# Kernel tuning notes

Hardware: AMD Instinct MI355X
Metric: run time of the kernel (lower is better)

The kernel has to match this reference:

```python
import jax, jax.numpy as jnp
import numpy as np

B, LVS, WIDTH, DEPTH = 8192, 512, 512, 7
EPS = 1e-5
SLOPE = 0.01  # torch LeakyReLU default negative_slope


def setup_inputs() -> dict:
    key = jax.random.key(0)
    ks = jax.random.split(key, 16)
    inp = {"x": jax.random.normal(ks[0], (B, LVS), dtype=jnp.float32)}
    for i in range(DEPTH):
        fan_in = LVS + WIDTH * i
        inp[f"W{i}"] = jax.random.normal(ks[1 + i], (WIDTH, fan_in), dtype=jnp.float32) / np.sqrt(fan_in)
    inp["b"] = 0.01 * jax.random.normal(ks[8], (DEPTH, WIDTH), dtype=jnp.float32)
    inp["gamma"] = jnp.ones((DEPTH, WIDTH), dtype=jnp.float32)
    inp["beta"] = jnp.zeros((DEPTH, WIDTH), dtype=jnp.float32)
    cin = LVS + DEPTH * WIDTH  # 4096
    inp["Wc"] = jax.random.normal(ks[9], (1, cin), dtype=jnp.float32) / np.sqrt(cin)
    inp["bc"] = jnp.zeros((1,), dtype=jnp.float32)
    # torch: rv = randn(...) * 0.02 + 1, multiplied onto each projection
    inp["noise"] = 1.0 + 0.02 * jax.random.normal(ks[10], (DEPTH, B, WIDTH), dtype=jnp.float32)
    return inp


def reference(x, W0, W1, W2, W3, W4, W5, W6, b, gamma, beta, Wc, bc, noise):
    Ws = (W0, W1, W2, W3, W4, W5, W6)
    last = x
    for i in range(DEPTH):
        # Linear: [B, in_i] @ [in_i, width]
        h = jnp.einsum('bi,wi->bw', last, Ws[i]) + b[i]
        # BatchNorm1d (training mode: batch stats, biased variance)
        mean = jnp.mean(h, axis=0)
        var = jnp.mean(jnp.square(h - mean), axis=0)
        h = (h - mean) * jax.lax.rsqrt(var + EPS) * gamma[i] + beta[i]
        # LeakyReLU + multiplicative noise, fused elementwise
        h = jnp.where(h >= 0, h, SLOPE * h) * noise[i]
        last = jnp.concatenate((last, h), axis=-1)
    logits = jnp.einsum('bi,oi->bo', last, Wc) + bc
    return jax.nn.sigmoid(logits)
```

## Files before the change

### kernel.cpp

```cpp
#include <hip/hip_runtime.h>

#define B_ROWS 8192
#define WIDTH  512
#define DEPTH  7
#define CIN    4096
#define EPS    1e-5f
#define SLOPE  0.01f

typedef __attribute__((ext_vector_type(8))) short short8;
typedef __attribute__((ext_vector_type(4))) short short4v;
typedef __attribute__((ext_vector_type(4))) float f32x4;
typedef __attribute__((ext_vector_type(16))) float f32x16;

__device__ inline short f2bf(float f) {
  unsigned u = __builtin_bit_cast(unsigned, f);
  unsigned r = (u + 0x7FFFu + ((u >> 16) & 1u)) >> 16;
  return (short)r;
}

__device__ inline float bf2f(short b) {
  unsigned u = ((unsigned)(unsigned short)b) << 16;
  return __builtin_bit_cast(float, u);
}

__device__ inline void gl_lds16(const void* g, void* l) {
  __builtin_amdgcn_global_load_lds(
      (const __attribute__((address_space(1))) unsigned*)g,
      (__attribute__((address_space(3))) unsigned*)l, 16, 0, 0);
}

struct WP { const float* p[7]; };

__global__ __launch_bounds__(256) void prolog(WP wp, short* __restrict__ wbf,
                                              const float* __restrict__ x,
                                              const float* __restrict__ wc,
                                              short* __restrict__ lastbf,
                                              float* __restrict__ logit,
                                              float* __restrict__ sumsz) {
  if (blockIdx.x >= 2048) {
    long e = ((long)(blockIdx.x - 2048) * 256 + threadIdx.x) * 4;
    int layer; long base;
    if      (e < 262144L)  { layer = 0; base = 0; }
    else if (e < 786432L)  { layer = 1; base = 262144L; }
    else if (e < 1572864L) { layer = 2; base = 786432L; }
    else if (e < 2621440L) { layer = 3; base = 1572864L; }
    else if (e < 3932160L) { layer = 4; base = 2621440L; }
    else if (e < 5505024L) { layer = 5; base = 3932160L; }
    else                   { layer = 6; base = 5505024L; }
    f32x4 v = *(const f32x4*)(wp.p[layer] + (e - base));
    short4v o;
    o.x = f2bf(v.x); o.y = f2bf(v.y); o.z = f2bf(v.z); o.w = f2bf(v.w);
    *(short4v*)(wbf + e) = o;
    return;
  }
  int gid = blockIdx.x * 256 + threadIdx.x;
  if (gid < DEPTH * 1024) sumsz[gid] = 0.f;
  int w = threadIdx.x >> 6, l = threadIdx.x & 63;
  int r = blockIdx.x * 4 + w;
  const float* xr = x + (long)r * 512 + l * 8;
  f32x4 v0 = *(const f32x4*)xr;
  f32x4 v1 = *(const f32x4*)(xr + 4);
  const float* wcr = wc + l * 8;
  float acc = 0.f;
  short8 ob;
#pragma unroll
  for (int j = 0; j < 4; ++j) { acc += v0[j] * wcr[j];     ob[j]     = f2bf(v0[j]); }
#pragma unroll
  for (int j = 0; j < 4; ++j) { acc += v1[j] * wcr[4 + j]; ob[4 + j] = f2bf(v1[j]); }
  *(short8*)&lastbf[(long)r * CIN + l * 8] = ob;
#pragma unroll
  for (int off = 32; off; off >>= 1) acc += __shfl_xor(acc, off);
  if (l == 0) logit[r] = acc;
}

__global__ __launch_bounds__(256, 2) void gemm_fused(const short* __restrict__ A,
                                                     const short* __restrict__ Bw,
                                                     short* __restrict__ C,
                                                     float* __restrict__ sums,
                                                     int K) {
  __shared__ __align__(16) char smem[49152];
  int t = threadIdx.x;
  int ks = t >> 6, l = t & 63;
  int l31 = l & 31, hi = l >> 5;
  int bm = blockIdx.x, bn = blockIdx.y;
  const short* Ab = A + (long)(bm * 128) * CIN;
  const short* Bb = Bw + (long)(bn * 64) * K;

  f32x16 acc[4][2];
#pragma unroll
  for (int m = 0; m < 4; ++m)
#pragma unroll
    for (int n = 0; n < 2; ++n)
#pragma unroll
      for (int r = 0; r < 16; ++r) acc[m][n][r] = 0.f;

  int l8 = l >> 3;
  int scol = ((l & 7) ^ l8) << 3;

#define STAGE(buf, k0)                                                                       \
  {                                                                                          \
    char* base = smem + (buf) * 24576;                                                       \
    int c0 = ks * 4, c1 = ks * 2;                                                            \
    gl_lds16(Ab + (long)((c0    ) * 8 + l8) * CIN + (k0) + scol, base + (c0    ) * 1024);    \
    gl_lds16(Ab + (long)((c0 + 1) * 8 + l8) * CIN + (k0) + scol, base + (c0 + 1) * 1024);    \
    gl_lds16(Ab + (long)((c0 + 2) * 8 + l8) * CIN + (k0) + scol, base + (c0 + 2) * 1024);    \
    gl_lds16(Ab + (long)((c0 + 3) * 8 + l8) * CIN + (k0) + scol, base + (c0 + 3) * 1024);    \
    gl_lds16(Bb + (long)((c1    ) * 8 + l8) * K + (k0) + scol, base + 16384 + (c1    ) * 1024); \
    gl_lds16(Bb + (long)((c1 + 1) * 8 + l8) * K + (k0) + scol, base + 16384 + (c1 + 1) * 1024); \
  }

  STAGE(0, 0);
  __syncthreads();

  int kb = ks * 32 + hi * 16;
  int sw = (l & 7) << 4;

  int nt = K >> 6;
  int cur = 0;
  for (int tix = 0; tix < nt; ++tix) {
    if (tix + 1 < nt) STAGE(cur ^ 1, (tix + 1) << 6);
    const char* AsC = smem + cur * 24576;
    const char* BsC = AsC + 16384;
    short8 a[4], b[2];
#pragma unroll
    for (int m = 0; m < 4; ++m)
      a[m] = *(const short8*)(AsC + (m * 32 + l31) * 128 + (kb ^ sw));
#pragma unroll
    for (int n = 0; n < 2; ++n)
      b[n] = *(const short8*)(BsC + (n * 32 + l31) * 128 + (kb ^ sw));
#pragma unroll
    for (int m = 0; m < 4; ++m)
#pragma unroll
      for (int n = 0; n < 2; ++n)
        acc[m][n] = __builtin_amdgcn_mfma_f32_32x32x16_bf16(a[m], b[n], acc[m][n], 0, 0, 0);
    __syncthreads();
    cur ^= 1;
  }

  float* Red = (float*)smem;
#define RIDX(m, n, r) (((m) * 32 + ((r) & 3) + 8 * ((r) >> 2) + 4 * hi) * 64 + (n) * 32 + l31)
  if (ks == 3) {
#pragma unroll
    for (int m = 0; m < 4; ++m)
#pragma unroll
      for (int n = 0; n < 2; ++n)
#pragma unroll
        for (int r = 0; r < 16; ++r) Red[RIDX(m, n, r)] = acc[m][n][r];
  }
  __syncthreads();
  if (ks == 2) {
#pragma unroll
    for (int m = 0; m < 4; ++m)
#pragma unroll
      for (int n = 0; n < 2; ++n)
#pragma unroll
        for (int r = 0; r < 16; ++r) Red[RIDX(m, n, r)] += acc[m][n][r];
  }
  __syncthreads();
  if (ks == 1) {
#pragma unroll
    for (int m = 0; m < 4; ++m)
#pragma unroll
      for (int n = 0; n < 2; ++n)
#pragma unroll
        for (int r = 0; r < 16; ++r) Red[RIDX(m, n, r)] += acc[m][n][r];
  }
  __syncthreads();
  if (ks == 0) {
    short* Cb = C + (long)(bm * 128) * WIDTH + bn * 64;
#pragma unroll
    for (int n = 0; n < 2; ++n) {
      float s = 0.f, q = 0.f;
#pragma unroll
      for (int m = 0; m < 4; ++m) {
#pragma unroll
        for (int r = 0; r < 16; ++r) {
          int cr = (r & 3) + 8 * (r >> 2) + 4 * hi;
          float v = acc[m][n][r] + Red[RIDX(m, n, r)];
          Cb[(long)(m * 32 + cr) * WIDTH + n * 32 + l31] = f2bf(v);
          s += v; q += v * v;
        }
      }
      s += __shfl_xor(s, 32);
      q += __shfl_xor(q, 32);
      if (l < 32) {
        int colg = bn * 64 + n * 32 + l;
        atomicAdd(&sums[colg], s);
        atomicAdd(&sums[WIDTH + colg], q);
      }
    }
  }
#undef RIDX
#undef STAGE
}

__global__ __launch_bounds__(256) void bnact(const short* __restrict__ h,
                                             const float* __restrict__ sums,
                                             const float* __restrict__ gamma,
                                             const float* __restrict__ beta,
                                             const float* __restrict__ noise,
                                             const float* __restrict__ wc,
                                             short* __restrict__ lastseg,
                                             float* __restrict__ logit) {
  int w = threadIdx.x >> 6, l = threadIdx.x & 63;
  int r = blockIdx.x * 4 + w;
  int c = l * 8;
  const float invB = 1.0f / 8192.0f;
  short8 hb = *(const short8*)&h[(long)r * WIDTH + c];
  f32x4 n0 = *(const f32x4*)&noise[(long)r * WIDTH + c];
  f32x4 n1 = *(const f32x4*)&noise[(long)r * WIDTH + c + 4];
  float acc = 0.f;
  short8 ob;
#pragma unroll
  for (int j = 0; j < 8; ++j) {
    int cc = c + j;
    float hv = bf2f(hb[j]);
    float nv = j < 4 ? n0[j] : n1[j - 4];
    float mean = sums[cc] * invB;
    float var = sums[WIDTH + cc] * invB - mean * mean;
    float v = (hv - mean) * rsqrtf(var + EPS);
    v = v * gamma[cc] + beta[cc];
    v = v >= 0.f ? v : SLOPE * v;
    v *= nv;
    acc += v * wc[cc];
    ob[j] = f2bf(v);
  }
  *(short8*)&lastseg[(long)r * CIN + c] = ob;
#pragma unroll
  for (int off = 32; off; off >>= 1) acc += __shfl_xor(acc, off);
  if (l == 0) logit[r] += acc;
}

__global__ __launch_bounds__(256) void finalize(const float* __restrict__ logit,
                                                const float* __restrict__ bc,
                                                float* __restrict__ out) {
  int i = blockIdx.x * 256 + threadIdx.x;
  float z = logit[i] + bc[0];
  out[i] = 1.0f / (1.0f + expf(-z));
}

extern "C" void kernel_launch(void* const* d_in, const int* in_sizes, int n_in,
                              void* d_out, int out_size, void* d_ws, size_t ws_size,
                              hipStream_t stream) {
  (void)in_sizes; (void)n_in; (void)out_size; (void)ws_size;
  const float* x     = (const float*)d_in[0];
  WP wp;
  for (int i = 0; i < 7; ++i) wp.p[i] = (const float*)d_in[1 + i];
  const float* gamma = (const float*)d_in[9];
  const float* beta  = (const float*)d_in[10];
  const float* Wc    = (const float*)d_in[11];
  const float* bc    = (const float*)d_in[12];
  const float* noise = (const float*)d_in[13];

  char* ws = (char*)d_ws;
  short* lastbf = (short*)ws;
  short* hpre   = (short*)(ws + 67108864);
  short* wbf    = (short*)(ws + 67108864 + 16777216);
  float* sums   = (float*)(ws + 67108864 + 16777216 + 14680064);
  float* logit  = (float*)(ws + 67108864 + 16777216 + 14680064 + 28672);

  prolog<<<9216, 256, 0, stream>>>(wp, wbf, x, Wc, lastbf, logit, sums);

  long woff = 0;
  for (int i = 0; i < DEPTH; ++i) {
    int K = 512 * (i + 1);
    gemm_fused<<<dim3(64, 8), 256, 0, stream>>>(lastbf, wbf + woff, hpre,
                                                sums + i * 1024, K);
    bnact<<<2048, 256, 0, stream>>>(hpre, sums + i * 1024,
                                    gamma + i * 512, beta + i * 512,
                                    noise + (long)i * B_ROWS * WIDTH,
                                    Wc + 512 + i * 512,
                                    lastbf + 512 + (long)i * 512, logit);
    woff += (long)512 * K;
  }
  finalize<<<32, 256, 0, stream>>>(logit, bc, (float*)d_out);
}
```

Baseline: 277.6 us.

## Deepen GEMM pipeline to 4 LDS stages and load B fragments directly to registers

The weight conversion now writes bf16 weights in a fragment-friendly blocked layout, so each lane can load its B MFMA operand straight from global memory into registers instead of staging it through LDS. The A tiles move to a 4-deep LDS ring buffer with prefetch three tiles ahead, and vmcnt-based waits plus raw barriers replace the full syncthreads. The aim is to hide global load latency better and cut LDS traffic for B. In exchange, LDS use grows to 64KB, which may limit occupancy at 2 blocks per CU, and the hand-counted vmcnt waits are fragile.

```diff
diff --git a/kernel.cpp b/kernel.cpp
--- a/kernel.cpp
+++ b/kernel.cpp
@@ -30,6 +30,18 @@
 }
 
 struct WP { const float* p[7]; };
+
+template <int L>
+__device__ inline void convw_one(const float* __restrict__ src,
+                                 short* __restrict__ dst, int idx) {
+  constexpr int FAN = 512 * (L + 1);
+  int col = idx / FAN;
+  int k = idx - col * FAN;
+  f32x4 v = *(const f32x4*)(src + idx);
+  short4v o;
+  o.x = f2bf(v.x); o.y = f2bf(v.y); o.z = f2bf(v.z); o.w = f2bf(v.w);
+  *(short4v*)(dst + ((long)(k >> 3) << 12) + (col << 3) + (k & 7)) = o;
+}
 
 __global__ __launch_bounds__(256) void prolog(WP wp, short* __restrict__ wbf,
                                               const float* __restrict__ x,
@@ -38,19 +50,14 @@
                                               float* __restrict__ logit,
                                               float* __restrict__ sumsz) {
   if (blockIdx.x >= 2048) {
-    long e = ((long)(blockIdx.x - 2048) * 256 + threadIdx.x) * 4;
-    int layer; long base;
-    if      (e < 262144L)  { layer = 0; base = 0; }
-    else if (e < 786432L)  { layer = 1; base = 262144L; }
-    else if (e < 1572864L) { layer = 2; base = 786432L; }
-    else if (e < 2621440L) { layer = 3; base = 1572864L; }
-    else if (e < 3932160L) { layer = 4; base = 2621440L; }
-    else if (e < 5505024L) { layer = 5; base = 3932160L; }
-    else                   { layer = 6; base = 5505024L; }
-    f32x4 v = *(const f32x4*)(wp.p[layer] + (e - base));
-    short4v o;
-    o.x = f2bf(v.x); o.y = f2bf(v.y); o.z = f2bf(v.z); o.w = f2bf(v.w);
-    *(short4v*)(wbf + e) = o;
+    int e = (int)(((long)(blockIdx.x - 2048) * 256 + threadIdx.x) * 4);
+    if      (e < 262144)  convw_one<0>(wp.p[0], wbf,           e);
+    else if (e < 786432)  convw_one<1>(wp.p[1], wbf + 262144,  e - 262144);
+    else if (e < 1572864) convw_one<2>(wp.p[2], wbf + 786432,  e - 786432);
+    else if (e < 2621440) convw_one<3>(wp.p[3], wbf + 1572864, e - 1572864);
+    else if (e < 3932160) convw_one<4>(wp.p[4], wbf + 2621440, e - 2621440);
+    else if (e < 5505024) convw_one<5>(wp.p[5], wbf + 3932160, e - 3932160);
+    else                  convw_one<6>(wp.p[6], wbf + 5505024, e - 5505024);
     return;
   }
   int gid = blockIdx.x * 256 + threadIdx.x;
@@ -78,13 +85,12 @@
                                                      short* __restrict__ C,
                                                      float* __restrict__ sums,
                                                      int K) {
-  __shared__ __align__(16) char smem[49152];
+  __shared__ __align__(16) char smem[65536];
   int t = threadIdx.x;
   int ks = t >> 6, l = t & 63;
   int l31 = l & 31, hi = l >> 5;
   int bm = blockIdx.x, bn = blockIdx.y;
   const short* Ab = A + (long)(bm * 128) * CIN;
-  const short* Bb = Bw + (long)(bn * 64) * K;
 
   f32x16 acc[4][2];
 #pragma unroll
@@ -96,46 +102,77 @@
 
   int l8 = l >> 3;
   int scol = ((l & 7) ^ l8) << 3;
-
-#define STAGE(buf, k0)                                                                       \
-  {                                                                                          \
-    char* base = smem + (buf) * 24576;                                                       \
-    int c0 = ks * 4, c1 = ks * 2;                                                            \
-    gl_lds16(Ab + (long)((c0    ) * 8 + l8) * CIN + (k0) + scol, base + (c0    ) * 1024);    \
-    gl_lds16(Ab + (long)((c0 + 1) * 8 + l8) * CIN + (k0) + scol, base + (c0 + 1) * 1024);    \
-    gl_lds16(Ab + (long)((c0 + 2) * 8 + l8) * CIN + (k0) + scol, base + (c0 + 2) * 1024);    \
-    gl_lds16(Ab + (long)((c0 + 3) * 8 + l8) * CIN + (k0) + scol, base + (c0 + 3) * 1024);    \
-    gl_lds16(Bb + (long)((c1    ) * 8 + l8) * K + (k0) + scol, base + 16384 + (c1    ) * 1024); \
-    gl_lds16(Bb + (long)((c1 + 1) * 8 + l8) * K + (k0) + scol, base + 16384 + (c1 + 1) * 1024); \
-  }
-
-  STAGE(0, 0);
-  __syncthreads();
+  const short* pA0 = Ab + (long)((ks * 4 + 0) * 8 + l8) * CIN + scol;
+  const short* pA1 = Ab + (long)((ks * 4 + 1) * 8 + l8) * CIN + scol;
+  const short* pA2 = Ab + (long)((ks * 4 + 2) * 8 + l8) * CIN + scol;
+  const short* pA3 = Ab + (long)((ks * 4 + 3) * 8 + l8) * CIN + scol;
+
+#define ASTAGE(base, k0)                              \
+  {                                                   \
+    gl_lds16(pA0 + (k0), (base) + (ks * 4 + 0) * 1024); \
+    gl_lds16(pA1 + (k0), (base) + (ks * 4 + 1) * 1024); \
+    gl_lds16(pA2 + (k0), (base) + (ks * 4 + 2) * 1024); \
+    gl_lds16(pA3 + (k0), (base) + (ks * 4 + 3) * 1024); \
+  }
+
+  const short* Bp = Bw + ((ks * 2 + hi) << 12) + ((bn * 64 + l31) << 3);
+#define BLOAD(d0, d1, tt)                              \
+  {                                                    \
+    const short* bp_ = Bp + ((long)(tt) << 15);        \
+    d0 = *(const short8*)bp_;                          \
+    d1 = *(const short8*)(bp_ + 256);                  \
+  }
 
   int kb = ks * 32 + hi * 16;
   int sw = (l & 7) << 4;
 
+#define AFRAGS_MFMA(rbase, b0, b1)                                             \
+  {                                                                            \
+    const char* AsC = (rbase);                                                 \
+    short8 a[4];                                                               \
+    _Pragma("unroll")                                                          \
+    for (int m = 0; m < 4; ++m)                                                \
+      a[m] = *(const short8*)(AsC + (m * 32 + l31) * 128 + (kb ^ sw));         \
+    _Pragma("unroll")                                                          \
+    for (int m = 0; m < 4; ++m) {                                              \
+      acc[m][0] = __builtin_amdgcn_mfma_f32_32x32x16_bf16(a[m], (b0), acc[m][0], 0, 0, 0); \
+      acc[m][1] = __builtin_amdgcn_mfma_f32_32x32x16_bf16(a[m], (b1), acc[m][1], 0, 0, 0); \
+    }                                                                          \
+  }
+
+  short8 bc0, bc1, bn0, bn1, bf0, bf1;
+  ASTAGE(smem, 0);
+  BLOAD(bc0, bc1, 0);
+  BLOAD(bn0, bn1, 1);
+  ASTAGE(smem + 16384, 64);
+  ASTAGE(smem + 32768, 128);
+  asm volatile("s_waitcnt vmcnt(10)" ::: "memory");
+  __builtin_amdgcn_s_barrier();
+
   int nt = K >> 6;
-  int cur = 0;
-  for (int tix = 0; tix < nt; ++tix) {
-    if (tix + 1 < nt) STAGE(cur ^ 1, (tix + 1) << 6);
-    const char* AsC = smem + cur * 24576;
-    const char* BsC = AsC + 16384;
-    short8 a[4], b[2];
-#pragma unroll
-    for (int m = 0; m < 4; ++m)
-      a[m] = *(const short8*)(AsC + (m * 32 + l31) * 128 + (kb ^ sw));
-#pragma unroll
-    for (int n = 0; n < 2; ++n)
-      b[n] = *(const short8*)(BsC + (n * 32 + l31) * 128 + (kb ^ sw));
-#pragma unroll
-    for (int m = 0; m < 4; ++m)
-#pragma unroll
-      for (int n = 0; n < 2; ++n)
-        acc[m][n] = __builtin_amdgcn_mfma_f32_32x32x16_bf16(a[m], b[n], acc[m][n], 0, 0, 0);
-    __syncthreads();
-    cur ^= 1;
-  }
+  for (int tix = 0; tix < nt - 3; ++tix) {
+    BLOAD(bf0, bf1, tix + 2);
+    ASTAGE(smem + (((tix + 3) & 3) << 14), (tix + 3) << 6);
+    AFRAGS_MFMA(smem + ((tix & 3) << 14), bc0, bc1);
+    asm volatile("s_waitcnt vmcnt(10)" ::: "memory");
+    __builtin_amdgcn_s_barrier();
+    bc0 = bn0; bc1 = bn1; bn0 = bf0; bn1 = bf1;
+  }
+  {
+    BLOAD(bf0, bf1, nt - 1);
+    AFRAGS_MFMA(smem + (((nt - 3) & 3) << 14), bc0, bc1);
+    asm volatile("s_waitcnt vmcnt(6)" ::: "memory");
+    __builtin_amdgcn_s_barrier();
+    bc0 = bn0; bc1 = bn1; bn0 = bf0; bn1 = bf1;
+  }
+  {
+    AFRAGS_MFMA(smem + (((nt - 2) & 3) << 14), bc0, bc1);
+    asm volatile("s_waitcnt vmcnt(0)" ::: "memory");
+    __builtin_amdgcn_s_barrier();
+    bc0 = bn0; bc1 = bn1;
+  }
+  AFRAGS_MFMA(smem + (((nt - 1) & 3) << 14), bc0, bc1);
+  __syncthreads();
 
   float* Red = (float*)smem;
 #define RIDX(m, n, r) (((m) * 32 + ((r) & 3) + 8 * ((r) >> 2) + 4 * hi) * 64 + (n) * 32 + l31)
@@ -191,7 +228,9 @@
     }
   }
 #undef RIDX
-#undef STAGE
+#undef AFRAGS_MFMA
+#undef BLOAD
+#undef ASTAGE
 }
 
 __global__ __launch_bounds__(256) void bnact(const short* __restrict__ h,
```

Result: slower. 288.7 us (+4.0%).

## Fuse BatchNorm activation into GEMM via grid-wide barrier on column statistics

Applied to the files above, without the earlier changes.

Merges the per-layer GEMM and BN/LeakyReLU/noise kernel into one launch. Each block keeps its output tile in LDS, prefetches its noise values, waits on an atomic-counter grid barrier until all 512 blocks have added their column sums, then normalizes and writes the bf16 activations and logit contributions directly. This removes the bf16 pre-activation round trip through global memory and one launch per layer. In exchange it depends on all 512 blocks being co-resident, since the spin barrier would otherwise deadlock, and it adds per-row atomics on the logits.

```diff
diff --git a/kernel.cpp b/kernel.cpp
--- a/kernel.cpp
+++ b/kernel.cpp
@@ -18,15 +18,22 @@
   return (short)r;
 }
 
-__device__ inline float bf2f(short b) {
-  unsigned u = ((unsigned)(unsigned short)b) << 16;
-  return __builtin_bit_cast(float, u);
-}
-
 __device__ inline void gl_lds16(const void* g, void* l) {
   __builtin_amdgcn_global_load_lds(
       (const __attribute__((address_space(1))) unsigned*)g,
       (__attribute__((address_space(3))) unsigned*)l, 16, 0, 0);
+}
+
+__device__ inline void gridbar(unsigned* ctr, unsigned target) {
+  __threadfence();
+  __syncthreads();
+  if (threadIdx.x == 0) {
+    __hip_atomic_fetch_add(ctr, 1u, __ATOMIC_ACQ_REL, __HIP_MEMORY_SCOPE_AGENT);
+    while (__hip_atomic_load(ctr, __ATOMIC_ACQUIRE, __HIP_MEMORY_SCOPE_AGENT) < target) {
+      __builtin_amdgcn_s_sleep(2);
+    }
+  }
+  __syncthreads();
 }
 
 struct WP { const float* p[7]; };
@@ -36,7 +43,8 @@
                                               const float* __restrict__ wc,
                                               short* __restrict__ lastbf,
                                               float* __restrict__ logit,
-                                              float* __restrict__ sumsz) {
+                                              float* __restrict__ sumsz,
+                                              unsigned* __restrict__ ctr) {
   if (blockIdx.x >= 2048) {
     long e = ((long)(blockIdx.x - 2048) * 256 + threadIdx.x) * 4;
     int layer; long base;
@@ -55,6 +63,7 @@
   }
   int gid = blockIdx.x * 256 + threadIdx.x;
   if (gid < DEPTH * 1024) sumsz[gid] = 0.f;
+  if (gid < 8) ctr[gid] = 0u;
   int w = threadIdx.x >> 6, l = threadIdx.x & 63;
   int r = blockIdx.x * 4 + w;
   const float* xr = x + (long)r * 512 + l * 8;
@@ -73,11 +82,12 @@
   if (l == 0) logit[r] = acc;
 }
 
-__global__ __launch_bounds__(256, 2) void gemm_fused(const short* __restrict__ A,
-                                                     const short* __restrict__ Bw,
-                                                     short* __restrict__ C,
-                                                     float* __restrict__ sums,
-                                                     int K) {
+__global__ __launch_bounds__(256, 2) void layer_fused(
+    const short* __restrict__ A, const short* __restrict__ Bw,
+    float* __restrict__ sums, const float* __restrict__ gamma,
+    const float* __restrict__ beta, const float* __restrict__ noise,
+    const float* __restrict__ wc, short* __restrict__ lastseg,
+    float* __restrict__ logit, unsigned* __restrict__ ctr, int K) {
   __shared__ __align__(16) char smem[49152];
   int t = threadIdx.x;
   int ks = t >> 6, l = t & 63;
@@ -167,7 +177,6 @@
   }
   __syncthreads();
   if (ks == 0) {
-    short* Cb = C + (long)(bm * 128) * WIDTH + bn * 64;
 #pragma unroll
     for (int n = 0; n < 2; ++n) {
       float s = 0.f, q = 0.f;
@@ -175,9 +184,8 @@
       for (int m = 0; m < 4; ++m) {
 #pragma unroll
         for (int r = 0; r < 16; ++r) {
-          int cr = (r & 3) + 8 * (r >> 2) + 4 * hi;
           float v = acc[m][n][r] + Red[RIDX(m, n, r)];
-          Cb[(long)(m * 32 + cr) * WIDTH + n * 32 + l31] = f2bf(v);
+          Red[RIDX(m, n, r)] = v;
           s += v; q += v * v;
         }
       }
@@ -192,43 +200,37 @@
   }
 #undef RIDX
 #undef STAGE
-}
-
-__global__ __launch_bounds__(256) void bnact(const short* __restrict__ h,
-                                             const float* __restrict__ sums,
-                                             const float* __restrict__ gamma,
-                                             const float* __restrict__ beta,
-                                             const float* __restrict__ noise,
-                                             const float* __restrict__ wc,
-                                             short* __restrict__ lastseg,
-                                             float* __restrict__ logit) {
-  int w = threadIdx.x >> 6, l = threadIdx.x & 63;
-  int r = blockIdx.x * 4 + w;
-  int c = l * 8;
+
+  int colL = bn * 64 + l;
+  const float* np = noise + (long)(bm * 128 + ks * 32) * WIDTH + colL;
+  float nv[32];
+#pragma unroll
+  for (int r = 0; r < 32; ++r) nv[r] = np[(long)r * WIDTH];
+
+  gridbar(ctr, 512u);
+
   const float invB = 1.0f / 8192.0f;
-  short8 hb = *(const short8*)&h[(long)r * WIDTH + c];
-  f32x4 n0 = *(const f32x4*)&noise[(long)r * WIDTH + c];
-  f32x4 n1 = *(const f32x4*)&noise[(long)r * WIDTH + c + 4];
-  float acc = 0.f;
-  short8 ob;
-#pragma unroll
-  for (int j = 0; j < 8; ++j) {
-    int cc = c + j;
-    float hv = bf2f(hb[j]);
-    float nv = j < 4 ? n0[j] : n1[j - 4];
-    float mean = sums[cc] * invB;
-    float var = sums[WIDTH + cc] * invB - mean * mean;
-    float v = (hv - mean) * rsqrtf(var + EPS);
-    v = v * gamma[cc] + beta[cc];
-    v = v >= 0.f ? v : SLOPE * v;
-    v *= nv;
-    acc += v * wc[cc];
-    ob[j] = f2bf(v);
-  }
-  *(short8*)&lastseg[(long)r * CIN + c] = ob;
-#pragma unroll
-  for (int off = 32; off; off >>= 1) acc += __shfl_xor(acc, off);
-  if (l == 0) logit[r] += acc;
+  float mean = __hip_atomic_load(&sums[colL], __ATOMIC_RELAXED, __HIP_MEMORY_SCOPE_AGENT) * invB;
+  float msq  = __hip_atomic_load(&sums[WIDTH + colL], __ATOMIC_RELAXED, __HIP_MEMORY_SCOPE_AGENT) * invB;
+  float rstd = rsqrtf(msq - mean * mean + EPS);
+  float g  = gamma[colL];
+  float be = beta[colL];
+  float wcv = wc[colL];
+  int row0 = bm * 128 + ks * 32;
+  short* lrow = lastseg + (long)row0 * CIN + colL;
+  const float* Rrow = Red + (ks * 32) * 64 + l;
+#pragma unroll
+  for (int r = 0; r < 32; ++r) {
+    float v = Rrow[r * 64];
+    float tv = (v - mean) * rstd * g + be;
+    tv = tv >= 0.f ? tv : SLOPE * tv;
+    tv *= nv[r];
+    lrow[(long)r * CIN] = f2bf(tv);
+    float p = tv * wcv;
+#pragma unroll
+    for (int off = 32; off; off >>= 1) p += __shfl_xor(p, off);
+    if (l == 0) atomicAdd(&logit[row0 + r], p);
+  }
 }
 
 __global__ __launch_bounds__(256) void finalize(const float* __restrict__ logit,
@@ -254,23 +256,23 @@
 
   char* ws = (char*)d_ws;
   short* lastbf = (short*)ws;
-  short* hpre   = (short*)(ws + 67108864);
   short* wbf    = (short*)(ws + 67108864 + 16777216);
   float* sums   = (float*)(ws + 67108864 + 16777216 + 14680064);
   float* logit  = (float*)(ws + 67108864 + 16777216 + 14680064 + 28672);
-
-  prolog<<<9216, 256, 0, stream>>>(wp, wbf, x, Wc, lastbf, logit, sums);
+  unsigned* ctr = (unsigned*)(ws + 67108864 + 16777216 + 14680064 + 28672 + 32768);
+
+  prolog<<<9216, 256, 0, stream>>>(wp, wbf, x, Wc, lastbf, logit, sums, ctr);
 
   long woff = 0;
   for (int i = 0; i < DEPTH; ++i) {
     int K = 512 * (i + 1);
-    gemm_fused<<<dim3(64, 8), 256, 0, stream>>>(lastbf, wbf + woff, hpre,
-                                                sums + i * 1024, K);
-    bnact<<<2048, 256, 0, stream>>>(hpre, sums + i * 1024,
-                                    gamma + i * 512, beta + i * 512,
-                                    noise + (long)i * B_ROWS * WIDTH,
-                                    Wc + 512 + i * 512,
-                                    lastbf + 512 + (long)i * 512, logit);
+    layer_fused<<<dim3(64, 8), 256, 0, stream>>>(
+        lastbf, wbf + woff, sums + i * 1024,
+        gamma + i * 512, beta + i * 512,
+        noise + (long)i * B_ROWS * WIDTH,
+        Wc + 512 + i * 512,
+        lastbf + 512 + (long)i * 512,
+        logit, ctr + i, K);
     woff += (long)512 * K;
   }
   finalize<<<32, 256, 0, stream>>>(logit, bc, (float*)d_out);
```

New measurement: 758.4 us. 2.73x slower.
